# Optimization experiments

Hardware: AMD Instinct MI355X
Metric: run time of the kernel (lower is better)

Reference implementation:

```python
import jax, jax.numpy as jnp
import numpy as np


def setup_inputs() -> dict:
    key = jax.random.key(0)
    k0, k1, k2, k3 = jax.random.split(key, 4)
    B, I, S = 4, 16, 4096      # batch, inDim, nSeq
    O, W = 64, 64
    T = 32768                  # nRealLen (output timeline length)
    x = jax.random.normal(k0, (B, I, S), dtype=jnp.float32)
    bound = float(np.sqrt(1.0 / (I * W)))  # torch uniform init of LTITRFGen
    weight = jax.random.uniform(k1, (O, I, W), dtype=jnp.float32, minval=-bound, maxval=bound)
    bias = jax.random.uniform(k2, (O,), dtype=jnp.float32, minval=-bound, maxval=bound)
    # strictly increasing, unique event onset indices per batch (scatter-set == scatter-add)
    stride = (T - W) // S  # = 7
    jitter = jax.random.randint(k3, (B, S), 0, stride)
    sourceIdx = (jnp.arange(S, dtype=jnp.int32)[None, :] * stride + jitter.astype(jnp.int32))
    return {"x": x, "weight": weight, "bias": bias, "sourceIdx": sourceIdx, "nRealLen": T}


def reference(x, weight, bias, sourceIdx, nRealLen):
    # x: (B, inDim, nSeq); weight: (outDim, inDim, nWin); bias: (outDim,)
    # sourceIdx: (B, nSeq) int, unique & sorted per batch; nRealLen: python int
    B, I, S = x.shape
    O, _, W = weight.shape
    # LTITRFGen (ifAddBiasInForward=False): sum over inDim of outer product
    trfs = jnp.einsum('bis,oiw->bows', x, weight)  # (B, O, W, S)
    # TRFAligner: scatter each TRF at its onset, then overlap-add (F.fold).
    # out[b, o, src[b,s] + w] += trfs[b, o, w, s]; trim to nRealLen.
    Tpad = nRealLen + W - 1
    tidx = sourceIdx[:, None, :] + jnp.arange(W, dtype=sourceIdx.dtype)[:, None]  # (B, W, S)

    def scatter_one(trf_b, tidx_b):
        # trf_b: (O, W, S), tidx_b: (W, S)
        return jnp.zeros((O, Tpad), dtype=trf_b.dtype).at[:, tidx_b.reshape(-1)].add(
            trf_b.reshape(O, -1))

    out = jax.vmap(scatter_one)(trfs, tidx)  # (B, O, Tpad)
    # ASTRF.forward adds the LTI bias per output channel
    return out[:, :, :nRealLen] + bias[:, None]
```

## Files before the change

kernel.cpp:

```cpp
#include <hip/hip_runtime.h>


#define BB   4
#define II   16
#define SS   4096
#define OO   64
#define WW   64
#define TLEN 32768
#define KK   1024
#define TT   256
#define YROWS 320
#define YPAD  24

typedef short bf16x8 __attribute__((ext_vector_type(8)));
typedef float f32x4  __attribute__((ext_vector_type(4)));

static __device__ __forceinline__ ushort f2bf(float f) {
    union { float f; uint u; } v; v.f = f;
    const uint u = v.u;
    return (ushort)((u + 0x7FFFu + ((u >> 16) & 1u)) >> 16);
}

__global__ void prep(const float* __restrict__ x, const float* __restrict__ w,
                     ushort* __restrict__ w3, ushort* __restrict__ xtb) {
    const int bid = blockIdx.x, tid = threadIdx.x;
    if (bid < 256) {
        const int idx  = bid * 256 + tid;
        const int j    = idx & 7;
        const int lane = (idx >> 3) & 63;
        const int n    = (idx >> 9) & 3;
        const int ks   = idx >> 11;
        const int nl = lane & 15, kg = lane >> 4;
        const int o  = n * 16 + nl;
        const int kk = ks * 32 + kg * 8 + j;
        const int i  = kk & 15, d = kk >> 4;
        w3[idx] = f2bf(w[o * KK + i * WW + d]);
        return;
    }
    __shared__ float tile[II][64 + 1];
    const int b = (bid - 256) >> 6, e0 = ((bid - 256) & 63) * 64;
    const int i = tid >> 6, el = tid & 63;
    #pragma unroll
    for (int k = 0; k < 4; ++k)
        tile[i + 4 * k][el] = x[((size_t)(b * II + i + 4 * k)) * SS + e0 + el];
    __syncthreads();
    const int e = tid >> 2, iq = tid & 3;
    ushort4 v;
    v.x = f2bf(tile[4 * iq + 0][e]);
    v.y = f2bf(tile[4 * iq + 1][e]);
    v.z = f2bf(tile[4 * iq + 2][e]);
    v.w = f2bf(tile[4 * iq + 3][e]);
    *(ushort4*)(xtb + ((size_t)(b * SS + e0 + e)) * II + iq * 4) = v;
}

__global__ __launch_bounds__(256, 2) void astrf_mfma(
    const ushort* __restrict__ w3,
    const ushort* __restrict__ xtb,
    const int*   __restrict__ srcIdx,
    const float* __restrict__ bias,
    float* __restrict__ out)
{
    __shared__ __align__(16) ushort yt[YROWS * YPAD];

    const int tid  = threadIdx.x;
    const int t0   = blockIdx.x * TT;
    const int b    = blockIdx.y;
    const int wave = tid >> 6, lane = tid & 63;
    const int nl   = lane & 15, kg = lane >> 4;

    uint4* z4 = (uint4*)yt;
    for (int c = tid; c < YROWS * YPAD / 8; c += 256)
        z4[c] = (uint4){0u, 0u, 0u, 0u};

    const int* sp = srcIdx + b * SS;
    const int tmin = t0 - (WW - 1);
    const int tmax = t0 + TT;
    int e_lo = tmin > 6 ? (tmin - 6) / 7 : 0;  if (e_lo > SS) e_lo = SS;
    while (e_lo > 0 && sp[e_lo - 1] >= tmin) --e_lo;
    while (e_lo < SS && sp[e_lo] < tmin) ++e_lo;
    int e_hi = tmax > 0 ? tmax / 7 : 0;  if (e_hi > SS) e_hi = SS;
    while (e_hi > 0 && sp[e_hi - 1] >= tmax) --e_hi;
    while (e_hi < SS && sp[e_hi] < tmax) ++e_hi;
    __syncthreads();

    {
        const int idx = tid >> 2, part = tid & 3;
        if (idx < e_hi - e_lo) {
            const int e = e_lo + idx;
            const int p = sp[e] - t0 + 63;
            const uint2 v = *(const uint2*)(xtb + ((size_t)(b * SS + e)) * II + part * 4);
            *(uint2*)&yt[p * YPAD + part * 4] = v;
        }
    }

    float bv[4];
    #pragma unroll
    for (int n = 0; n < 4; ++n) bv[n] = bias[n * 16 + nl];
    const int abase = (wave * 64 + nl + 63 - (kg >> 1)) * YPAD + (kg & 1) * 8;
    const ushort* wl = w3 + lane * 8;

    __syncthreads();

    f32x4 acc[4][4];
    #pragma unroll
    for (int mi = 0; mi < 4; ++mi)
        #pragma unroll
        for (int n = 0; n < 4; ++n)
            acc[mi][n] = (f32x4){0.f, 0.f, 0.f, 0.f};

    bf16x8 A[2][4], Bf[2][4];
    #pragma unroll
    for (int mi = 0; mi < 4; ++mi) A[0][mi] = *(const bf16x8*)&yt[abase + mi * 16 * YPAD];
    #pragma unroll
    for (int n = 0; n < 4; ++n)   Bf[0][n] = *(const bf16x8*)(wl + n * 512);

    #pragma unroll
    for (int ks = 0; ks < 32; ++ks) {
        const int cu = ks & 1, nx = cu ^ 1;
        if (ks < 31) {
            #pragma unroll
            for (int mi = 0; mi < 4; ++mi)
                A[nx][mi] = *(const bf16x8*)&yt[abase - (ks + 1) * 2 * YPAD + mi * 16 * YPAD];
            #pragma unroll
            for (int n = 0; n < 4; ++n)
                Bf[nx][n] = *(const bf16x8*)(wl + ((ks + 1) * 4 + n) * 512);
        }
        #pragma unroll
        for (int n = 0; n < 4; ++n)
            #pragma unroll
            for (int mi = 0; mi < 4; ++mi)
                acc[mi][n] = __builtin_amdgcn_mfma_f32_16x16x32_bf16(
                    A[cu][mi], Bf[cu][n], acc[mi][n], 0, 0, 0);
    }

    #pragma unroll
    for (int mi = 0; mi < 4; ++mi) {
        const int t = t0 + wave * 64 + mi * 16 + kg * 4;
        #pragma unroll
        for (int n = 0; n < 4; ++n) {
            const int o = n * 16 + nl;
            float4 v;
            v.x = acc[mi][n][0] + bv[n];
            v.y = acc[mi][n][1] + bv[n];
            v.z = acc[mi][n][2] + bv[n];
            v.w = acc[mi][n][3] + bv[n];
            *(float4*)(out + ((size_t)(b * OO + o)) * TLEN + t) = v;
        }
    }
}

extern "C" void kernel_launch(void* const* d_in, const int* in_sizes, int n_in,
                              void* d_out, int out_size, void* d_ws, size_t ws_size,
                              hipStream_t stream) {
    const float* x    = (const float*)d_in[0];
    const float* wgt  = (const float*)d_in[1];
    const float* bias = (const float*)d_in[2];
    const int*   src  = (const int*)d_in[3];
    float* out = (float*)d_out;

    ushort* w3  = (ushort*)d_ws;
    ushort* xtb = (ushort*)((char*)d_ws + 131072);

    prep<<<dim3(512), 256, 0, stream>>>(x, wgt, w3, xtb);
    astrf_mfma<<<dim3(TLEN / TT, BB), 256, 0, stream>>>(w3, xtb, src, bias, out);
}
```

Baseline: 107.7 us.

## Stage shared weight fragments in double-buffered LDS via global_load_lds

Previously every wave read the full bf16 weight matrix from global memory straight into registers, so each block fetched the same weights four times. The weights are now copied once per block into a double-buffered LDS area with the async global_load_lds builtin, prefetching the next 16 KB stage while MFMAs consume the current one. Waves then read B fragments from LDS. This adds 32 KB of LDS per block and a block barrier per stage, which may reduce occupancy headroom and add sync stalls.

```diff
diff --git a/kernel.cpp b/kernel.cpp
--- a/kernel.cpp
+++ b/kernel.cpp
@@ -14,6 +14,8 @@
 
 typedef short bf16x8 __attribute__((ext_vector_type(8)));
 typedef float f32x4  __attribute__((ext_vector_type(4)));
+typedef __attribute__((address_space(3))) void       lds_void;
+typedef __attribute__((address_space(1))) const void gbl_void;
 
 static __device__ __forceinline__ ushort f2bf(float f) {
     union { float f; uint u; } v; v.f = f;
@@ -61,6 +63,7 @@
     float* __restrict__ out)
 {
     __shared__ __align__(16) ushort yt[YROWS * YPAD];
+    __shared__ __align__(16) ushort bw[2][8192];
 
     const int tid  = threadIdx.x;
     const int t0   = blockIdx.x * TT;
@@ -93,13 +96,19 @@
         }
     }
 
+    const char* w3b = (const char*)w3;
+    #pragma unroll
+    for (int j = 0; j < 4; ++j) {
+        const void* g = w3b + (wave * 4 + j) * 1024 + lane * 16;
+        __builtin_amdgcn_global_load_lds((gbl_void*)g,
+                                         (lds_void*)&bw[0][(wave * 4 + j) * 512],
+                                         16, 0, 0);
+    }
+
     float bv[4];
     #pragma unroll
     for (int n = 0; n < 4; ++n) bv[n] = bias[n * 16 + nl];
     const int abase = (wave * 64 + nl + 63 - (kg >> 1)) * YPAD + (kg & 1) * 8;
-    const ushort* wl = w3 + lane * 8;
-
-    __syncthreads();
 
     f32x4 acc[4][4];
     #pragma unroll
@@ -108,29 +117,38 @@
         for (int n = 0; n < 4; ++n)
             acc[mi][n] = (f32x4){0.f, 0.f, 0.f, 0.f};
 
-    bf16x8 A[2][4], Bf[2][4];
-    #pragma unroll
-    for (int mi = 0; mi < 4; ++mi) A[0][mi] = *(const bf16x8*)&yt[abase + mi * 16 * YPAD];
-    #pragma unroll
-    for (int n = 0; n < 4; ++n)   Bf[0][n] = *(const bf16x8*)(wl + n * 512);
+    __syncthreads();
 
     #pragma unroll
-    for (int ks = 0; ks < 32; ++ks) {
-        const int cu = ks & 1, nx = cu ^ 1;
-        if (ks < 31) {
+    for (int p = 0; p < 8; ++p) {
+        const int buf = p & 1;
+        if (p < 7) {
+            #pragma unroll
+            for (int j = 0; j < 4; ++j) {
+                const void* g = w3b + (p + 1) * 16384 + (wave * 4 + j) * 1024 + lane * 16;
+                __builtin_amdgcn_global_load_lds((gbl_void*)g,
+                                                 (lds_void*)&bw[buf ^ 1][(wave * 4 + j) * 512],
+                                                 16, 0, 0);
+            }
+        }
+        #pragma unroll
+        for (int ksl = 0; ksl < 4; ++ksl) {
+            const int ks = p * 4 + ksl;
+            bf16x8 A[4], Bf[4];
             #pragma unroll
             for (int mi = 0; mi < 4; ++mi)
-                A[nx][mi] = *(const bf16x8*)&yt[abase - (ks + 1) * 2 * YPAD + mi * 16 * YPAD];
+                A[mi] = *(const bf16x8*)&yt[abase - ks * 2 * YPAD + mi * 16 * YPAD];
             #pragma unroll
             for (int n = 0; n < 4; ++n)
-                Bf[nx][n] = *(const bf16x8*)(wl + ((ks + 1) * 4 + n) * 512);
+                Bf[n] = *(const bf16x8*)&bw[buf][(ksl * 4 + n) * 512 + lane * 8];
+            #pragma unroll
+            for (int n = 0; n < 4; ++n)
+                #pragma unroll
+                for (int mi = 0; mi < 4; ++mi)
+                    acc[mi][n] = __builtin_amdgcn_mfma_f32_16x16x32_bf16(
+                        A[mi], Bf[n], acc[mi][n], 0, 0, 0);
         }
-        #pragma unroll
-        for (int n = 0; n < 4; ++n)
-            #pragma unroll
-            for (int mi = 0; mi < 4; ++mi)
-                acc[mi][n] = __builtin_amdgcn_mfma_f32_16x16x32_bf16(
-                    A[cu][mi], Bf[cu][n], acc[mi][n], 0, 0, 0);
+        __syncthreads();
     }
 
     #pragma unroll
```

Result: faster. 89.25 us (-17.2%).
